# Performance work log

Measured on AMD Instinct MI355X. Metric: run time of the kernel, lower is better.

Reference implementation:

```python
import jax, jax.numpy as jnp
import numpy as np

NUM_HEADS = 8


def setup_inputs() -> dict:
    key = jax.random.key(0)
    ks = jax.random.split(key, 10)
    B, L, D, H = 2, 2048, 512, NUM_HEADS
    Pd = D // H
    s = 1.0 / np.sqrt(D)
    return {
        "x": jax.random.normal(ks[0], (B, L, D), jnp.float32),
        "Wq": jax.random.normal(ks[1], (D, D), jnp.float32) * s,
        "bq": jnp.zeros((D,), jnp.float32),
        "Wk": jax.random.normal(ks[2], (D, D), jnp.float32) * s,
        "bk": jnp.zeros((D,), jnp.float32),
        "Wv": jax.random.normal(ks[3], (D, D), jnp.float32) * s,
        "bv": jnp.zeros((D,), jnp.float32),
        "Wo": jax.random.normal(ks[4], (D, D), jnp.float32) * s,
        "bo": jnp.zeros((D,), jnp.float32),
        "E": jax.random.normal(ks[5], (L, Pd), jnp.float32) * (1.0 / np.sqrt(Pd)),
    }


def reference(x, Wq, bq, Wk, bk, Wv, bv, Wo, bo, E):
    B, L, D = x.shape
    H = NUM_HEADS
    Pd = D // H

    def split_heads(t):
        return t.reshape(B, L, H, Pd).transpose(0, 2, 1, 3)  # [B,H,L,Pd]

    q = split_heads(x @ Wq + bq)
    k = split_heads(x @ Wk + bk)
    v = split_heads(x @ Wv + bv)

    # relative attention: QE matmul + upper-triangular-style mask + skew
    QE = jnp.einsum('bhld,md->bhlm', q, E)  # [B,H,L,M] with M == max_seq == L
    M = QE.shape[-1]
    i = jnp.arange(L)[:, None]
    j = jnp.arange(M)[None, :]
    # row l keeps positions j >= M-1-l (logical_not of sequence_mask with lengths M-1-l)
    qe_mask = (j >= (M - 1 - i)).astype(QE.dtype)
    QE = QE * qe_mask
    # skewing trick: pad a zero column on the left, reshape swapping last two dims, drop first row
    padded = jnp.pad(QE, ((0, 0), (0, 0), (0, 0), (1, 0)))  # [B,H,L,M+1]
    rel = padded.reshape(B, H, M + 1, L)[:, :, 1:, :]        # [B,H,L,L]

    score = jnp.einsum('bhld,bhmd->bhlm', q, k) + rel
    scaled = score / jnp.sqrt(jnp.asarray(Pd, jnp.float32))

    # causal mask: i >= j - n_src + n_dest, with n_src == n_dest == L -> i >= j
    cmask = (jnp.arange(L)[:, None] >= jnp.arange(L)[None, :]).astype(scaled.dtype)
    scaled = scaled * cmask - 10000.0 * (1.0 - cmask)

    weights = jax.nn.softmax(scaled, axis=-1)
    attn = jnp.einsum('bhlm,bhmd->bhld', weights, v)
    attn = attn.transpose(0, 2, 1, 3).reshape(B, L, D)
    return attn @ Wo + bo
```

## Files before the change

kernel.cpp:

```cpp
#include <hip/hip_runtime.h>
#include <hip/hip_bf16.h>

typedef __attribute__((ext_vector_type(8))) short short8;
typedef __attribute__((ext_vector_type(4))) short short4_;
typedef __attribute__((ext_vector_type(4))) float f32x4;

#define MFMA16(a,b,c) __builtin_amdgcn_mfma_f32_16x16x32_bf16(a,b,c,0,0,0)

#define QSC 0.18033688011112042f
#define MASKVAL -14427.0f

__device__ __forceinline__ ushort f2b(float f){
  union { float f; unsigned u; } v; v.f = f;
  unsigned u = v.u;
  unsigned r = (u + 0x7FFFu + ((u >> 16) & 1u)) >> 16;
  return (ushort)r;
}
__device__ __forceinline__ float b2f(ushort u){
  union { unsigned u; float f; } v; v.u = ((unsigned)u) << 16; return v.f;
}

__global__ void cvt_all(const float* __restrict__ x, const float* __restrict__ E,
                        ushort* __restrict__ xb, ushort* __restrict__ ebuf){
  int i = (blockIdx.x*256 + threadIdx.x)*4;
  const float* src; ushort* dst; int off;
  if (i < 2097152){ src = x; dst = xb; off = i; }
  else            { src = E; dst = ebuf; off = i - 2097152; }
  float4 v = *(const float4*)(src + off);
  short4_ o;
  o[0]=(short)f2b(v.x); o[1]=(short)f2b(v.y); o[2]=(short)f2b(v.z); o[3]=(short)f2b(v.w);
  *(short4_*)(dst + off) = o;
}

__global__ void transpose_cvt4(const float* __restrict__ Wq, const float* __restrict__ Wk,
                               const float* __restrict__ Wv, const float* __restrict__ Wo,
                               ushort* __restrict__ wtall, ushort* __restrict__ wot){
  int z = blockIdx.z;
  const float* in = (z==0) ? Wq : (z==1) ? Wk : (z==2) ? Wv : Wo;
  ushort* out = (z<3) ? (wtall + z*262144) : wot;
  __shared__ float t[64][65];
  int r0 = blockIdx.y*64, c0 = blockIdx.x*64;
  int tr = threadIdx.x>>4, tc = (threadIdx.x&15)*4;
  #pragma unroll
  for (int i=0;i<4;i++){
    float4 v = *(const float4*)(in + (r0 + tr + i*16)*512 + c0 + tc);
    t[tr+i*16][tc+0]=v.x; t[tr+i*16][tc+1]=v.y; t[tr+i*16][tc+2]=v.z; t[tr+i*16][tc+3]=v.w;
  }
  __syncthreads();
  #pragma unroll
  for (int i=0;i<4;i++){
    int orow = tr + i*16;
    short4_ o;
    #pragma unroll
    for (int e=0;e<4;e++) o[e] = (short)f2b(t[tc+e][orow]);
    *(short4_*)(out + (c0+orow)*512 + r0 + tc) = o;
  }
}

__global__ __launch_bounds__(256) void gemm_qkv(
    const ushort* __restrict__ xb, const ushort* __restrict__ wt,
    const float* __restrict__ bq, const float* __restrict__ bk, const float* __restrict__ bv,
    ushort* __restrict__ qo, ushort* __restrict__ ko, ushort* __restrict__ vo){
  __shared__ float tbuf[64][65];
  int lane = threadIdx.x & 63, w = threadIdx.x >> 6;
  int g = lane >> 4, c = lane & 15;
  int m0 = blockIdx.y*64, n0 = blockIdx.x*64;
  const ushort* ap = xb + (m0 + w*16 + c)*512 + g*8;
  f32x4 acc[4] = {{0,0,0,0},{0,0,0,0},{0,0,0,0},{0,0,0,0}};
  #pragma unroll 4
  for (int k0=0;k0<512;k0+=32){
    short8 a = *(const short8*)(ap + k0);
    #pragma unroll
    for (int t=0;t<4;t++){
      short8 b = *(const short8*)(wt + (n0 + t*16 + c)*512 + k0 + g*8);
      acc[t] = MFMA16(a,b,acc[t]);
    }
  }
  int which = n0 >> 9;
  int d0 = n0 & 511;
  if (which < 2){
    const float* bias = (which==0) ? bq : bk;
    ushort* dst = (which==0) ? qo : ko;
    float scl = (which==0) ? QSC : 1.0f;
    #pragma unroll
    for (int t=0;t<4;t++){
      int d = d0 + t*16 + c;
      float bs = bias[d];
      int h = d >> 6, pd = d & 63;
      #pragma unroll
      for (int rr=0;rr<4;rr++){
        int m = m0 + w*16 + g*4 + rr;
        int b_ = m >> 11, lrow = m & 2047;
        dst[(((b_<<3)+h)*2048 + lrow)*64 + pd] = f2b((acc[t][rr] + bs)*scl);
      }
    }
  } else {
    #pragma unroll
    for (int t=0;t<4;t++){
      float bs = bv[d0 + t*16 + c];
      #pragma unroll
      for (int rr=0;rr<4;rr++) tbuf[t*16+c][w*16 + g*4 + rr] = acc[t][rr] + bs;
    }
    __syncthreads();
    int pdr = threadIdx.x >> 2, lseg = (threadIdx.x & 3) << 4;
    int b_ = m0 >> 11, h = d0 >> 6;
    ushort* dst = vo + (((b_<<3) + h)*64 + pdr)*2048 + (m0 & 2047) + lseg;
    short8 o0, o1;
    #pragma unroll
    for (int e=0;e<8;e++){ o0[e] = (short)f2b(tbuf[pdr][lseg+e]); o1[e] = (short)f2b(tbuf[pdr][lseg+8+e]); }
    *(short8*)(dst)   = o0;
    *(short8*)(dst+8) = o1;
  }
}

__global__ __launch_bounds__(256) void gemm_o(
    const ushort* __restrict__ ab, const ushort* __restrict__ wot,
    const float* __restrict__ bo, float* __restrict__ out){
  int lane = threadIdx.x & 63, w = threadIdx.x >> 6;
  int g = lane >> 4, c = lane & 15;
  int m0 = blockIdx.y*64, n0 = blockIdx.x*64;
  const ushort* ap = ab + (m0 + w*16 + c)*512 + g*8;
  f32x4 acc[4] = {{0,0,0,0},{0,0,0,0},{0,0,0,0},{0,0,0,0}};
  #pragma unroll 4
  for (int k0=0;k0<512;k0+=32){
    short8 a = *(const short8*)(ap + k0);
    #pragma unroll
    for (int t=0;t<4;t++){
      short8 b = *(const short8*)(wot + (n0 + t*16 + c)*512 + k0 + g*8);
      acc[t] = MFMA16(a,b,acc[t]);
    }
  }
  #pragma unroll
  for (int t=0;t<4;t++){
    int n = n0 + t*16 + c;
    float bs = bo[n];
    #pragma unroll
    for (int rr=0;rr<4;rr++){
      int m = m0 + w*16 + g*4 + rr;
      out[m*512 + n] = acc[t][rr] + bs;
    }
  }
}

__global__ __launch_bounds__(256,4) void attn_rel(
    const ushort* __restrict__ q, const ushort* __restrict__ k,
    const ushort* __restrict__ vtg, const ushort* __restrict__ eb,
    ushort* __restrict__ partO, float* __restrict__ partml){
  int gid = blockIdx.x;
  int bh = gid / 144;
  int u  = gid - bh*144;
  int m = 0;
  #pragma unroll
  for (int t=0;t<7;t++) if (u >= 2*(m+1)*(m+2)) m++;
  int rem = u - 2*m*(m+1);
  int qi = 4*m + rem/(m+1);
  int ch = rem - (qi-4*m)*(m+1);
  int ntt = qi + 1 - ch*4; if (ntt > 4) ntt = 4;
  int i0 = qi << 6;
  int tid = threadIdx.x, lane = tid&63, w = tid>>6, g = lane>>4, c = lane&15;
  const ushort* Q  = q   + bh*131072;
  const ushort* K  = k   + bh*131072;
  const ushort* VT = vtg + bh*131072;
  int iw = i0 + w*16;

  __shared__ ushort pl[4][16][72];
  __shared__ ushort vt[2][8][64][8];

  short8 qa0 = *(const short8*)(Q + (iw + c)*64 + g*8);
  short8 qa1 = *(const short8*)(Q + (iw + c)*64 + 32 + g*8);

  int sd = tid >> 2;
  int q2 = (tid & 3) << 1;
  const ushort* vsrc = VT + sd*2048 + (q2<<3);
  int j0base = ch << 8;

  {
    short8 a = *(const short8*)(vsrc + j0base);
    short8 b = *(const short8*)(vsrc + j0base + 8);
    *(short8*)(&vt[0][q2  ][sd][0]) = a;
    *(short8*)(&vt[0][q2+1][sd][0]) = b;
  }
  __syncthreads();

  f32x4 oacc[4] = {{0,0,0,0},{0,0,0,0},{0,0,0,0},{0,0,0,0}};
  float m_run[4] = {-1e30f,-1e30f,-1e30f,-1e30f};
  float l_run[4] = {0.f,0.f,0.f,0.f};
  short8 vra, vrb;

  for (int tt=0; tt<ntt; ++tt){
    int j0 = j0base + (tt<<6);
    int curb = tt & 1;
    bool pf = (tt+1 < ntt);
    if (pf){
      vra = *(const short8*)(vsrc + j0 + 64);
      vrb = *(const short8*)(vsrc + j0 + 64 + 8);
    }
    f32x4 s[4];
    #pragma unroll
    for (int t=0;t<4;t++){
      const ushort* kp = K + (j0 + t*16 + c)*64 + g*8;
      short8 kf0 = *(const short8*)(kp);
      short8 kf1 = *(const short8*)(kp + 32);
      f32x4 z = {0,0,0,0};
      z = MFMA16(qa0, kf0, z);
      z = MFMA16(qa1, kf1, z);
      s[t] = z;
    }
    int r0 = 2032 - iw + j0;
    f32x4 zb[5];
    #pragma unroll
    for (int t=0;t<5;t++){
      int r = r0 + t*16 + c; if (r > 2047) r = 2047;
      const ushort* ep = eb + r*64 + g*8;
      short8 ef0 = *(const short8*)(ep);
      short8 ef1 = *(const short8*)(ep + 32);
      f32x4 z = {0,0,0,0};
      z = MFMA16(qa0, ef0, z);
      z = MFMA16(qa1, ef1, z);
      zb[t] = z;
    }
    float sv[4][4];
    #pragma unroll
    for (int rr=0;rr<4;rr++){
      int qrow = g*4 + rr;
      int srcl = (lane & 48) | ((c + 15 - qrow) & 15);
      float shv[5];
      #pragma unroll
      for (int t=0;t<5;t++) shv[t] = __shfl(zb[t][rr], srcl, 64);
      bool hi = (c > qrow);
      #pragma unroll
      for (int tS=0;tS<4;tS++){
        int jg = j0 + tS*16 + c;
        float relv = hi ? shv[tS+1] : shv[tS];
        float val = s[tS][rr] + relv;
        sv[tS][rr] = (jg > iw + qrow) ? MASKVAL : val;
      }
    }
    float al[4];
    #pragma unroll
    for (int rr=0;rr<4;rr++){
      float mx = fmaxf(fmaxf(sv[0][rr],sv[1][rr]), fmaxf(sv[2][rr],sv[3][rr]));
      #pragma unroll
      for (int off=1; off<16; off<<=1) mx = fmaxf(mx, __shfl_xor(mx, off));
      float mn = fmaxf(m_run[rr], mx);
      al[rr] = exp2f(m_run[rr] - mn);
      m_run[rr] = mn;
    }
    #pragma unroll
    for (int rr=0;rr<4;rr++){
      float sum = 0.f;
      #pragma unroll
      for (int t=0;t<4;t++){
        float p = exp2f(sv[t][rr] - m_run[rr]);
        sum += p;
        pl[w][g*4+rr][t*16+c] = f2b(p);
      }
      #pragma unroll
      for (int off=1; off<16; off<<=1) sum += __shfl_xor(sum, off);
      l_run[rr] = l_run[rr]*al[rr] + sum;
    }
    #pragma unroll
    for (int d=0;d<4;d++){
      #pragma unroll
      for (int rr=0;rr<4;rr++) oacc[d][rr] *= al[rr];
    }
    short8 pa0 = *(const short8*)(&pl[w][c][g*8]);
    short8 pa1 = *(const short8*)(&pl[w][c][32 + g*8]);
    #pragma unroll
    for (int d=0;d<4;d++){
      short8 vb0 = *(const short8*)(&vt[curb][g  ][d*16+c][0]);
      short8 vb1 = *(const short8*)(&vt[curb][g+4][d*16+c][0]);
      oacc[d] = MFMA16(pa0, vb0, oacc[d]);
      oacc[d] = MFMA16(pa1, vb1, oacc[d]);
    }
    if (pf){
      *(short8*)(&vt[curb^1][q2  ][sd][0]) = vra;
      *(short8*)(&vt[curb^1][q2+1][sd][0]) = vrb;
    }
    __syncthreads();
  }

  int pb = gid;
  #pragma unroll
  for (int rr=0;rr<4;rr++){
    int row = w*16 + g*4 + rr;
    #pragma unroll
    for (int d=0;d<4;d++){
      partO[pb*4096 + row*64 + d*16 + c] = f2b(oacc[d][rr]);
    }
    if (c == 0){
      partml[pb*128 + row]      = m_run[rr];
      partml[pb*128 + 64 + row] = l_run[rr];
    }
  }
}

__global__ __launch_bounds__(256) void attn_merge(
    const ushort* __restrict__ partO, const float* __restrict__ partml,
    ushort* __restrict__ attn){
  int qi = blockIdx.x;
  int bh = blockIdx.y;
  int m = qi >> 2, rq = qi & 3;
  int nch = m + 1;
  int cb0 = 2*m*(m+1) + rq*(m+1);
  int tid = threadIdx.x;
  int r = tid>>2, seg = (tid&3)<<4;
  int pbase = bh*144 + cb0;
  float M = -1e30f;
  for (int s=0;s<nch;s++) M = fmaxf(M, partml[(pbase+s)*128 + r]);
  float lf = 0.f;
  float acc[16];
  #pragma unroll
  for (int e=0;e<16;e++) acc[e] = 0.f;
  for (int s=0;s<nch;s++){
    float ms = partml[(pbase+s)*128 + r];
    float ls = partml[(pbase+s)*128 + 64 + r];
    float ww = exp2f(ms - M);
    lf += ww*ls;
    const ushort* op = partO + (pbase+s)*4096 + r*64 + seg;
    short8 o0 = *(const short8*)(op);
    short8 o1 = *(const short8*)(op + 8);
    #pragma unroll
    for (int e=0;e<8;e++){
      acc[e]   += ww*b2f((ushort)o0[e]);
      acc[8+e] += ww*b2f((ushort)o1[e]);
    }
  }
  float inv = 1.f/lf;
  int b_ = bh>>3, h = bh&7;
  ushort* dst = attn + ((b_*2048 + (qi<<6) + r)*8 + h)*64 + seg;
  short8 r0, r1;
  #pragma unroll
  for (int e=0;e<8;e++){ r0[e] = (short)f2b(acc[e]*inv); r1[e] = (short)f2b(acc[8+e]*inv); }
  *(short8*)(dst)   = r0;
  *(short8*)(dst+8) = r1;
}


extern "C" void kernel_launch(void* const* d_in, const int* in_sizes, int n_in,
                              void* d_out, int out_size, void* d_ws, size_t ws_size,
                              hipStream_t stream){
  const float* x  = (const float*)d_in[0];
  const float* Wq = (const float*)d_in[1];
  const float* bq = (const float*)d_in[2];
  const float* Wk = (const float*)d_in[3];
  const float* bk = (const float*)d_in[4];
  const float* Wv = (const float*)d_in[5];
  const float* bv = (const float*)d_in[6];
  const float* Wo = (const float*)d_in[7];
  const float* bo = (const float*)d_in[8];
  const float* E  = (const float*)d_in[9];
  float* out = (float*)d_out;

  ushort* ws    = (ushort*)d_ws;
  ushort* xb    = ws;
  ushort* wtall = xb    + 2097152;
  ushort* wot   = wtall + 786432;
  ushort* ebuf  = wot   + 262144;
  ushort* qb    = ebuf  + 131072;
  ushort* kb    = qb    + 2097152;
  ushort* vb2   = kb    + 2097152;
  ushort* ab    = vb2   + 2097152;
  ushort* partO = ab    + 2097152;
  float*  partml= (float*)(partO + 9437184);

  cvt_all<<<2176, 256, 0, stream>>>(x, E, xb, ebuf);
  transpose_cvt4<<<dim3(8,8,4), 256, 0, stream>>>(Wq, Wk, Wv, Wo, wtall, wot);
  gemm_qkv<<<dim3(24,64), 256, 0, stream>>>(xb, wtall, bq, bk, bv, qb, kb, vb2);
  attn_rel<<<2304, 256, 0, stream>>>(qb, kb, vb2, ebuf, partO, partml);
  attn_merge<<<dim3(32,16), 256, 0, stream>>>(partO, partml, ab);
  gemm_o<<<dim3(8,64), 256, 0, stream>>>(ab, wot, bo, out);
}
```

Measured before the change: 265.2 us.

## Stage GEMM tiles in LDS via direct global-to-LDS loads with larger block tiles

```diff
diff --git a/kernel.cpp b/kernel.cpp
--- a/kernel.cpp
+++ b/kernel.cpp
@@ -18,6 +18,10 @@
 }
 __device__ __forceinline__ float b2f(ushort u){
   union { unsigned u; float f; } v; v.u = ((unsigned)u) << 16; return v.f;
+}
+__device__ __forceinline__ void gload16(const ushort* g, ushort* l){
+  __builtin_amdgcn_global_load_lds((const __attribute__((address_space(1))) unsigned int*)g,
+                                   (__attribute__((address_space(3))) unsigned int*)l, 16, 0, 0);
 }
 
 __global__ void cvt_all(const float* __restrict__ x, const float* __restrict__ E,
@@ -61,21 +65,44 @@
     const ushort* __restrict__ xb, const ushort* __restrict__ wt,
     const float* __restrict__ bq, const float* __restrict__ bk, const float* __restrict__ bv,
     ushort* __restrict__ qo, ushort* __restrict__ ko, ushort* __restrict__ vo){
-  __shared__ float tbuf[64][65];
-  int lane = threadIdx.x & 63, w = threadIdx.x >> 6;
-  int g = lane >> 4, c = lane & 15;
-  int m0 = blockIdx.y*64, n0 = blockIdx.x*64;
-  const ushort* ap = xb + (m0 + w*16 + c)*512 + g*8;
-  f32x4 acc[4] = {{0,0,0,0},{0,0,0,0},{0,0,0,0},{0,0,0,0}};
-  #pragma unroll 4
+  __shared__ ushort smem[8192];
+  ushort* As = smem;
+  ushort* Bs = smem + 4096;
+  int tid = threadIdx.x, lane = tid&63, w = tid>>6, g = lane>>4, c = lane&15;
+  int wr = w>>1, wc = w&1;
+  int m0 = blockIdx.y*128, n0 = blockIdx.x*128;
+  int srow = lane>>2, scol = (lane&3)*8;
+  const ushort* a0 = xb + (m0 + w*32 + srow)*512 + scol;
+  const ushort* a1 = a0 + 16*512;
+  const ushort* b0 = wt + (n0 + w*32 + srow)*512 + scol;
+  const ushort* b1 = b0 + 16*512;
+  ushort* la = As + w*1024;
+  ushort* lb = Bs + w*1024;
+
+  f32x4 acc[4][4];
+  #pragma unroll
+  for (int i=0;i<4;i++)
+    #pragma unroll
+    for (int j=0;j<4;j++) acc[i][j] = (f32x4){0,0,0,0};
+
   for (int k0=0;k0<512;k0+=32){
-    short8 a = *(const short8*)(ap + k0);
-    #pragma unroll
-    for (int t=0;t<4;t++){
-      short8 b = *(const short8*)(wt + (n0 + t*16 + c)*512 + k0 + g*8);
-      acc[t] = MFMA16(a,b,acc[t]);
-    }
-  }
+    if (k0) __syncthreads();
+    gload16(a0 + k0, la);
+    gload16(a1 + k0, la + 512);
+    gload16(b0 + k0, lb);
+    gload16(b1 + k0, lb + 512);
+    __syncthreads();
+    short8 af[4], bf[4];
+    #pragma unroll
+    for (int mi=0;mi<4;mi++) af[mi] = *(const short8*)(As + (wr*64 + mi*16 + c)*32 + g*8);
+    #pragma unroll
+    for (int ni=0;ni<4;ni++) bf[ni] = *(const short8*)(Bs + (wc*64 + ni*16 + c)*32 + g*8);
+    #pragma unroll
+    for (int mi=0;mi<4;mi++)
+      #pragma unroll
+      for (int ni=0;ni<4;ni++) acc[mi][ni] = MFMA16(af[mi], bf[ni], acc[mi][ni]);
+  }
+
   int which = n0 >> 9;
   int d0 = n0 & 511;
   if (which < 2){
@@ -83,61 +110,103 @@
     ushort* dst = (which==0) ? qo : ko;
     float scl = (which==0) ? QSC : 1.0f;
     #pragma unroll
-    for (int t=0;t<4;t++){
-      int d = d0 + t*16 + c;
+    for (int ni=0;ni<4;ni++){
+      int d = d0 + wc*64 + ni*16 + c;
       float bs = bias[d];
       int h = d >> 6, pd = d & 63;
       #pragma unroll
-      for (int rr=0;rr<4;rr++){
-        int m = m0 + w*16 + g*4 + rr;
-        int b_ = m >> 11, lrow = m & 2047;
-        dst[(((b_<<3)+h)*2048 + lrow)*64 + pd] = f2b((acc[t][rr] + bs)*scl);
+      for (int mi=0;mi<4;mi++){
+        #pragma unroll
+        for (int rr=0;rr<4;rr++){
+          int m = m0 + wr*64 + mi*16 + g*4 + rr;
+          int b_ = m >> 11, lrow = m & 2047;
+          dst[(((b_<<3)+h)*2048 + lrow)*64 + pd] = f2b((acc[mi][ni][rr] + bs)*scl);
+        }
       }
     }
   } else {
-    #pragma unroll
-    for (int t=0;t<4;t++){
-      float bs = bv[d0 + t*16 + c];
-      #pragma unroll
-      for (int rr=0;rr<4;rr++) tbuf[t*16+c][w*16 + g*4 + rr] = acc[t][rr] + bs;
-    }
-    __syncthreads();
-    int pdr = threadIdx.x >> 2, lseg = (threadIdx.x & 3) << 4;
-    int b_ = m0 >> 11, h = d0 >> 6;
-    ushort* dst = vo + (((b_<<3) + h)*64 + pdr)*2048 + (m0 & 2047) + lseg;
-    short8 o0, o1;
-    #pragma unroll
-    for (int e=0;e<8;e++){ o0[e] = (short)f2b(tbuf[pdr][lseg+e]); o1[e] = (short)f2b(tbuf[pdr][lseg+8+e]); }
-    *(short8*)(dst)   = o0;
-    *(short8*)(dst+8) = o1;
+    ushort (*tb)[72] = (ushort (*)[72])smem;
+    int b_ = m0 >> 11;
+    #pragma unroll
+    for (int r=0;r<4;r++){
+      __syncthreads();
+      if (w == r){
+        #pragma unroll
+        for (int ni=0;ni<4;ni++){
+          float bs = bv[d0 + wc*64 + ni*16 + c];
+          #pragma unroll
+          for (int mi=0;mi<4;mi++){
+            short4_ pk;
+            #pragma unroll
+            for (int rr=0;rr<4;rr++) pk[rr] = (short)f2b(acc[mi][ni][rr] + bs);
+            *(short4_*)(&tb[ni*16 + c][mi*16 + g*4]) = pk;
+          }
+        }
+      }
+      __syncthreads();
+      int qr = r>>1, qc = r&1;
+      int pd = tid>>2, lseg = (tid&3)<<4;
+      short8 v0 = *(const short8*)(&tb[pd][lseg]);
+      short8 v1 = *(const short8*)(&tb[pd][lseg+8]);
+      int dg = d0 + qc*64 + pd;
+      int hh = dg>>6, pdl = dg&63;
+      ushort* dst = vo + (((b_<<3)+hh)*64 + pdl)*2048 + (m0 & 2047) + qr*64 + lseg;
+      *(short8*)(dst)   = v0;
+      *(short8*)(dst+8) = v1;
+    }
   }
 }
 
 __global__ __launch_bounds__(256) void gemm_o(
     const ushort* __restrict__ ab, const ushort* __restrict__ wot,
     const float* __restrict__ bo, float* __restrict__ out){
-  int lane = threadIdx.x & 63, w = threadIdx.x >> 6;
-  int g = lane >> 4, c = lane & 15;
-  int m0 = blockIdx.y*64, n0 = blockIdx.x*64;
-  const ushort* ap = ab + (m0 + w*16 + c)*512 + g*8;
-  f32x4 acc[4] = {{0,0,0,0},{0,0,0,0},{0,0,0,0},{0,0,0,0}};
-  #pragma unroll 4
+  __shared__ ushort smem[6144];
+  ushort* As = smem;
+  ushort* Bs = smem + 2048;
+  int tid = threadIdx.x, lane = tid&63, w = tid>>6, g = lane>>4, c = lane&15;
+  int wr = w>>1, wc = w&1;
+  int m0 = blockIdx.y*64, n0 = blockIdx.x*128;
+  int srow = lane>>2, scol = (lane&3)*8;
+  const ushort* a0 = ab  + (m0 + w*16 + srow)*512 + scol;
+  const ushort* b0 = wot + (n0 + w*32 + srow)*512 + scol;
+  const ushort* b1 = b0 + 16*512;
+  ushort* la = As + w*512;
+  ushort* lb = Bs + w*1024;
+
+  f32x4 acc[2][4];
+  #pragma unroll
+  for (int i=0;i<2;i++)
+    #pragma unroll
+    for (int j=0;j<4;j++) acc[i][j] = (f32x4){0,0,0,0};
+
   for (int k0=0;k0<512;k0+=32){
-    short8 a = *(const short8*)(ap + k0);
-    #pragma unroll
-    for (int t=0;t<4;t++){
-      short8 b = *(const short8*)(wot + (n0 + t*16 + c)*512 + k0 + g*8);
-      acc[t] = MFMA16(a,b,acc[t]);
-    }
-  }
-  #pragma unroll
-  for (int t=0;t<4;t++){
-    int n = n0 + t*16 + c;
+    if (k0) __syncthreads();
+    gload16(a0 + k0, la);
+    gload16(b0 + k0, lb);
+    gload16(b1 + k0, lb + 512);
+    __syncthreads();
+    short8 af[2], bf[4];
+    #pragma unroll
+    for (int mi=0;mi<2;mi++) af[mi] = *(const short8*)(As + (wr*32 + mi*16 + c)*32 + g*8);
+    #pragma unroll
+    for (int ni=0;ni<4;ni++) bf[ni] = *(const short8*)(Bs + (wc*64 + ni*16 + c)*32 + g*8);
+    #pragma unroll
+    for (int mi=0;mi<2;mi++)
+      #pragma unroll
+      for (int ni=0;ni<4;ni++) acc[mi][ni] = MFMA16(af[mi], bf[ni], acc[mi][ni]);
+  }
+
+  #pragma unroll
+  for (int ni=0;ni<4;ni++){
+    int n = n0 + wc*64 + ni*16 + c;
     float bs = bo[n];
     #pragma unroll
-    for (int rr=0;rr<4;rr++){
-      int m = m0 + w*16 + g*4 + rr;
-      out[m*512 + n] = acc[t][rr] + bs;
+    for (int mi=0;mi<2;mi++){
+      #pragma unroll
+      for (int rr=0;rr<4;rr++){
+        int m = m0 + wr*32 + mi*16 + g*4 + rr;
+        out[m*512 + n] = acc[mi][ni][rr] + bs;
+      }
     }
   }
 }
@@ -366,8 +435,8 @@
 
   cvt_all<<<2176, 256, 0, stream>>>(x, E, xb, ebuf);
   transpose_cvt4<<<dim3(8,8,4), 256, 0, stream>>>(Wq, Wk, Wv, Wo, wtall, wot);
-  gemm_qkv<<<dim3(24,64), 256, 0, stream>>>(xb, wtall, bq, bk, bv, qb, kb, vb2);
+  gemm_qkv<<<dim3(12,32), 256, 0, stream>>>(xb, wtall, bq, bk, bv, qb, kb, vb2);
   attn_rel<<<2304, 256, 0, stream>>>(qb, kb, vb2, ebuf, partO, partml);
   attn_merge<<<dim3(32,16), 256, 0, stream>>>(partO, partml, ab);
-  gemm_o<<<dim3(8,64), 256, 0, stream>>>(ab, wot, bo, out);
-}
+  gemm_o<<<dim3(4,64), 256, 0, stream>>>(ab, wot, bo, out);
+}
```

New measurement: 215.1 us. 1.23x faster.
